# Kernel tuning notes

Measured on AMD Instinct MI355X. Metric: run time of the kernel, lower is better.

The kernel has to match this reference:

```python
import jax, jax.numpy as jnp
import numpy as np

B, L, D, H, F, NL = 112, 128, 768, 12, 3072, 3
E = D // H  # head dim = 64
BN_EPS = 1e-5


def _bn(x, gamma, beta):
    # torch BatchNorm1d applied on x.permute(0,2,1): per-channel (d_model) stats over batch+seq
    mean = jnp.mean(x, axis=(0, 1), keepdims=True)
    var = jnp.var(x, axis=(0, 1), keepdims=True)
    return (x - mean) * jax.lax.rsqrt(var + BN_EPS) * gamma + beta


def setup_inputs() -> dict:
    key = jax.random.key(0)
    ks = jax.random.split(key, 10)
    s = 0.02
    inp = {
        "x": jax.random.normal(ks[0], (B, L, D), jnp.float32),
        "attn_bias": jax.random.normal(ks[1], (B, L, L, H), jnp.float32) * 0.1,
        "Wq": jax.random.normal(ks[2], (NL, D, D), jnp.float32) * s,
        "bq": jnp.zeros((NL, D), jnp.float32),
        "Wk": jax.random.normal(ks[3], (NL, D, D), jnp.float32) * s,
        "bk": jnp.zeros((NL, D), jnp.float32),
        "Wv": jax.random.normal(ks[4], (NL, D, D), jnp.float32) * s,
        "bv": jnp.zeros((NL, D), jnp.float32),
        "Wo": jax.random.normal(ks[5], (NL, D, D), jnp.float32) * s,
        "bo": jnp.zeros((NL, D), jnp.float32),
        "W1": jax.random.normal(ks[6], (NL, F, D), jnp.float32) * s,  # conv1 k=1 == Linear
        "b1": jnp.zeros((NL, F), jnp.float32),
        "W2": jax.random.normal(ks[7], (NL, D, F), jnp.float32) * s,  # conv2 k=1 == Linear
        "b2": jnp.zeros((NL, D), jnp.float32),
        "g1": jnp.ones((NL, D), jnp.float32),
        "be1": jnp.zeros((NL, D), jnp.float32),
        "g2": jnp.ones((NL, D), jnp.float32),
        "be2": jnp.zeros((NL, D), jnp.float32),
        "gf": jnp.ones((D,), jnp.float32),
        "bef": jnp.zeros((D,), jnp.float32),
    }
    return inp


def reference(x, attn_bias, Wq, bq, Wk, bk, Wv, bv, Wo, bo,
              W1, b1, W2, b2, g1, be1, g2, be2, gf, bef):
    scale = 1.0 / float(np.sqrt(E))
    bias_bhls = jnp.transpose(attn_bias, (0, 3, 1, 2))  # [B,H,L,S]
    for l in range(NL):
        q = (x @ Wq[l].T + bq[l]).reshape(B, L, H, E)
        k = (x @ Wk[l].T + bk[l]).reshape(B, L, H, E)
        v = (x @ Wv[l].T + bv[l]).reshape(B, L, H, E)
        scores = jnp.einsum('blhe,bshe->bhls', q, k)  # O(L^2) score tensor
        A = jax.nn.softmax(scores * scale + bias_bhls, axis=-1)
        V = jnp.einsum('bhls,bshd->blhd', A, v).reshape(B, L, D)
        new_x = V @ Wo[l].T + bo[l]
        x = _bn(x + new_x, g1[l], be1[l])
        y = jax.nn.gelu(x @ W1[l].T + b1[l], approximate=False)
        y = y @ W2[l].T + b2[l]
        x = _bn(x + y, g2[l], be2[l])
    return _bn(x, gf, bef)  # Encoder final BatchNorm1d(d_model)
```

## Files before the change

### kernel.cpp

```cpp
#include <hip/hip_runtime.h>

#define NB 112
#define SEQ 128
#define DM 768
#define NH 12
#define HD 64
#define FF 3072
#define NLAYER 3
#define MTOK (NB*SEQ)
#define QKVN (3*DM)
#define HEADTOT (NB*NH)
#define QSZ ((size_t)HEADTOT*SEQ*HD)

typedef unsigned short u16;
typedef __attribute__((ext_vector_type(8))) short short8;
typedef __attribute__((ext_vector_type(4))) float f32x4;
typedef __attribute__((ext_vector_type(4))) unsigned short us4;

__device__ __forceinline__ u16 f2bf(float f){
  unsigned u = __builtin_bit_cast(unsigned, f);
  u += 0x7FFFu + ((u >> 16) & 1u);
  return (u16)(u >> 16);
}
__device__ __forceinline__ float bf2f(u16 b){
  unsigned u = ((unsigned)b) << 16;
  return __builtin_bit_cast(float, u);
}

__device__ __forceinline__ void gl_lds16(const void* g, void* l){
  __builtin_amdgcn_global_load_lds((const __attribute__((address_space(1))) unsigned*)g,
                                   (__attribute__((address_space(3))) unsigned*)l, 16, 0, 0);
}

template<int EPI>
__global__ __launch_bounds__(512, 2)
void gemm_bt(const u16* __restrict__ A, const u16* __restrict__ W,
             const float* __restrict__ bias, u16* __restrict__ obf,
             float* __restrict__ of32, const float* __restrict__ res,
             float* __restrict__ p1, float* __restrict__ p2,
             int M, int N, int K, int Nt, int TPB)
{
  __shared__ __align__(16) char smem[131072];
  const int tid = threadIdx.x;
  const int w = tid >> 6, lane = tid & 63;
  const int wm = w >> 2, wn = w & 3;
  const int fr = lane & 15, fg = lane >> 4;
  const int fko = fg * 8;
  const int grid = gridDim.x;
  const int q8 = grid >> 3, r8 = grid & 7;
  const int xcd = blockIdx.x & 7, pos = blockIdx.x >> 3;
  const int start = xcd < r8 ? xcd * (q8 + 1) : r8 * (q8 + 1) + (xcd - r8) * q8;
  const int swz = start + pos;
  const int nt = K >> 6;
  const int tot = TPB * nt;
  const int l3 = lane >> 3;
  const int k16s = ((lane & 7) ^ l3) * 8;
  int rowAK[2][2], rowBK[2][2];
  #pragma unroll
  for (int mh = 0; mh < 2; mh++)
    #pragma unroll
    for (int j = 0; j < 2; j++)
      rowAK[mh][j] = (mh*64 + j*128 + w*8 + l3) * K;
  #pragma unroll
  for (int h = 0; h < 2; h++)
    #pragma unroll
    for (int j = 0; j < 2; j++)
      rowBK[h][j] = (h*128 + (w + j*8)*8 + l3) * K;

  auto stA2 = [&](int bb, int mh, int soff) {
    const u16* g0 = A + (size_t)soff + rowAK[mh][0] + k16s;
    const u16* g1 = A + (size_t)soff + rowAK[mh][1] + k16s;
    char* d = smem + bb*65536 + (mh*64 + w*8)*128;
    gl_lds16(g0, d);
    gl_lds16(g1, d + 16384);
  };
  auto stB2 = [&](int bb, int h, int soff) {
    const u16* g0 = W + (size_t)soff + rowBK[h][0] + k16s;
    const u16* g1 = W + (size_t)soff + rowBK[h][1] + k16s;
    char* d = smem + bb*65536 + 32768 + (h*128 + w*8)*128;
    gl_lds16(g0, d);
    gl_lds16(g1, d + 8192);
  };
  const int axor = (fr & 7) << 4;
  auto rdA2 = [&](int bb, int mh, int kh, int mf) -> short8 {
    const int row = wm*128 + mh*64 + mf*16 + fr;
    return *(const short8*)(smem + bb*65536 + row*128 + (((kh*32 + fko)*2) ^ axor));
  };
  auto rdB2 = [&](int bb, int kh, int nf) -> short8 {
    const int row = wn*64 + nf*16 + fr;
    return *(const short8*)(smem + bb*65536 + 32768 + row*128 + (((kh*32 + fko)*2) ^ axor));
  };
  auto coord = [&](int r, int& bm, int& bn) {
    const int lin = swz * TPB + r;
    const int mI = lin / Nt;
    bm = mI * 256; bn = (lin - mI * Nt) * 256;
  };

  f32x4 acc[8][4] = {};

  auto epi = [&](int bm, int bn) {
    float bs[4] = {0,0,0,0}, bq[4] = {0,0,0,0};
    #pragma unroll
    for (int mi = 0; mi < 8; mi++) {
      #pragma unroll
      for (int ni = 0; ni < 4; ni++) {
        const int c = bn + wn*64 + ni*16 + fr;
        const int r0 = bm + wm*128 + (mi>>2)*64 + (mi&3)*16 + fg*4;
        const float bc = bias[c];
        #pragma unroll
        for (int j = 0; j < 4; j++) {
          float v = acc[mi][ni][j] + bc;
          const int r = r0 + j;
          if constexpr (EPI == 1) {
            v = 0.5f * v * (1.0f + erff(v * 0.70710678118654752f));
            obf[(size_t)r * N + c] = f2bf(v);
          } else if constexpr (EPI == 2) {
            const float y = v + res[(size_t)r * N + c];
            of32[(size_t)r * N + c] = y;
            bs[ni] += y; bq[ni] += y * y;
          } else {
            const int which = c / DM;
            const int cc = c - which * DM;
            const int hh = cc >> 6, e = cc & 63;
            const int bb = r >> 7, l = r & 127;
            obf[(size_t)which * QSZ + ((size_t)(bb*NH + hh) * SEQ + l) * HD + e] = f2bf(v);
          }
        }
        acc[mi][ni] = (f32x4){0.f, 0.f, 0.f, 0.f};
      }
    }
    if constexpr (EPI == 2) {
      const int mIdx = bm >> 8;
      #pragma unroll
      for (int ni = 0; ni < 4; ni++) {
        float s = bs[ni], qq = bq[ni];
        s  += __shfl_xor(s, 16);  s  += __shfl_xor(s, 32);
        qq += __shfl_xor(qq, 16); qq += __shfl_xor(qq, 32);
        if (fg == 0) {
          const int c = bn + wn*64 + ni*16 + fr;
          p1[(mIdx*2 + wm) * N + c] = s;
          p2[(mIdx*2 + wm) * N + c] = qq;
        }
      }
    }
  };

  int r0 = 0, kt0 = 0, bm0, bn0; coord(0, bm0, bn0);
  int r1 = 0, kt1 = 1, bm1 = bm0, bn1 = bn0;
  int r2 = 0, kt2 = 2, bm2 = bm0;
  if (kt2 >= nt) { kt2 -= nt; r2 = 1; int d; if (r2 < TPB) coord(r2, bm2, d); }

  stA2(0, 0, bm0*K); stA2(0, 1, bm0*K);
  stB2(0, 0, bn0*K); stB2(0, 1, bn0*K);
  if (tot > 1) stA2(1, 0, bm1*K + kt1*64);
  asm volatile("s_waitcnt vmcnt(2)" ::: "memory");
  __builtin_amdgcn_s_barrier();

  short8 bk0[4], bk1[4], av[4];
  for (int it = 0; it < tot; ++it) {
    const int bufc = it & 1, nb = bufc ^ 1;
    const bool st1 = (it + 1 < tot), st2 = (it + 2 < tot);
    const int sB1 = bn1*K + kt1*64;
    const int sA1 = bm1*K + kt1*64;
    const int sA2 = bm2*K + kt2*64;
    #pragma unroll
    for (int i = 0; i < 4; i++) av[i] = rdA2(bufc, 0, 0, i);
    #pragma unroll
    for (int i = 0; i < 4; i++) bk0[i] = rdB2(bufc, 0, i);
    if (st1) stB2(nb, 0, sB1);
    __builtin_amdgcn_s_barrier();
    asm volatile("s_waitcnt lgkmcnt(0)" ::: "memory");
    __builtin_amdgcn_sched_barrier(0);
    __builtin_amdgcn_s_setprio(1);
    #pragma unroll
    for (int mi = 0; mi < 4; mi++)
      #pragma unroll
      for (int ni = 0; ni < 4; ni++)
        acc[mi][ni] = __builtin_amdgcn_mfma_f32_16x16x32_bf16(av[mi], bk0[ni], acc[mi][ni], 0, 0, 0);
    __builtin_amdgcn_s_setprio(0);
    __builtin_amdgcn_s_barrier();
    #pragma unroll
    for (int i = 0; i < 4; i++) av[i] = rdA2(bufc, 0, 1, i);
    #pragma unroll
    for (int i = 0; i < 4; i++) bk1[i] = rdB2(bufc, 1, i);
    if (st1) stB2(nb, 1, sB1);
    __builtin_amdgcn_s_barrier();
    asm volatile("s_waitcnt lgkmcnt(0)" ::: "memory");
    __builtin_amdgcn_sched_barrier(0);
    __builtin_amdgcn_s_setprio(1);
    #pragma unroll
    for (int mi = 0; mi < 4; mi++)
      #pragma unroll
      for (int ni = 0; ni < 4; ni++)
        acc[mi][ni] = __builtin_amdgcn_mfma_f32_16x16x32_bf16(av[mi], bk1[ni], acc[mi][ni], 0, 0, 0);
    __builtin_amdgcn_s_setprio(0);
    if (st1) { asm volatile("s_waitcnt vmcnt(4)" ::: "memory"); }
    else     { asm volatile("s_waitcnt vmcnt(0)" ::: "memory"); }
    __builtin_amdgcn_s_barrier();
    #pragma unroll
    for (int i = 0; i < 4; i++) av[i] = rdA2(bufc, 1, 0, i);
    if (st2) stA2(bufc, 0, sA2);
    __builtin_amdgcn_s_barrier();
    asm volatile("s_waitcnt lgkmcnt(0)" ::: "memory");
    __builtin_amdgcn_sched_barrier(0);
    __builtin_amdgcn_s_setprio(1);
    #pragma unroll
    for (int mi = 0; mi < 4; mi++)
      #pragma unroll
      for (int ni = 0; ni < 4; ni++)
        acc[4+mi][ni] = __builtin_amdgcn_mfma_f32_16x16x32_bf16(av[mi], bk0[ni], acc[4+mi][ni], 0, 0, 0);
    __builtin_amdgcn_s_setprio(0);
    __builtin_amdgcn_s_barrier();
    #pragma unroll
    for (int i = 0; i < 4; i++) av[i] = rdA2(bufc, 1, 1, i);
    if (st1) stA2(nb, 1, sA1);
    __builtin_amdgcn_s_barrier();
    asm volatile("s_waitcnt lgkmcnt(0)" ::: "memory");
    __builtin_amdgcn_sched_barrier(0);
    __builtin_amdgcn_s_setprio(1);
    #pragma unroll
    for (int mi = 0; mi < 4; mi++)
      #pragma unroll
      for (int ni = 0; ni < 4; ni++)
        acc[4+mi][ni] = __builtin_amdgcn_mfma_f32_16x16x32_bf16(av[mi], bk1[ni], acc[4+mi][ni], 0, 0, 0);
    __builtin_amdgcn_s_setprio(0);
    if (st2)      { asm volatile("s_waitcnt vmcnt(4)" ::: "memory"); }
    else if (st1) { asm volatile("s_waitcnt vmcnt(2)" ::: "memory"); }
    __builtin_amdgcn_s_barrier();
    if (kt0 == nt - 1) {
      epi(bm0, bn0);
      kt0 = 0; r0++;
      if (r0 < TPB) coord(r0, bm0, bn0);
    } else kt0++;
    kt1++; if (kt1 == nt) { kt1 = 0; r1++; if (r1 < TPB) coord(r1, bm1, bn1); }
    kt2++; if (kt2 == nt) { kt2 = 0; r2++; if (r2 < TPB) { int d; coord(r2, bm2, d); } }
  }
}

__global__ __launch_bounds__(256)
void attn_kernel(const u16* __restrict__ qkvb, const u16* __restrict__ biasT,
                 u16* __restrict__ ab)
{
  const int h = blockIdx.x, b = blockIdx.y;
  const int tid = threadIdx.x, w = tid >> 6, lane = tid & 63;
  const int bh = b * NH + h;
  const u16* qp = qkvb + (size_t)bh * SEQ * HD;
  const u16* kp = qkvb + QSZ + (size_t)bh * SEQ * HD;
  const u16* vp = qkvb + 2 * QSZ + (size_t)bh * SEQ * HD;
  __shared__ __align__(16) u16 vT[HD * 136];
  __shared__ __align__(16) u16 P[SEQ * 136];
  {
    const int s = tid & 127, half = tid >> 7;
    #pragma unroll
    for (int rr = 0; rr < 4; rr++) {
      const int e0 = half * 32 + rr * 8;
      short8 v8 = *(const short8*)&vp[s * HD + e0];
      #pragma unroll
      for (int j = 0; j < 8; j++) vT[(e0 + j) * 136 + s] = (u16)v8[j];
    }
  }
  const int fr = lane & 15, fg = lane >> 4;
  f32x4 sacc[2][8] = {};
  #pragma unroll
  for (int ks = 0; ks < 2; ks++) {
    const int k0 = ks * 32 + fg * 8;
    short8 qf[2], kf[8];
    #pragma unroll
    for (int mi = 0; mi < 2; mi++) qf[mi] = *(const short8*)&qp[(w*32 + mi*16 + fr) * HD + k0];
    #pragma unroll
    for (int ni = 0; ni < 8; ni++) kf[ni] = *(const short8*)&kp[(ni*16 + fr) * HD + k0];
    #pragma unroll
    for (int mi = 0; mi < 2; mi++)
      #pragma unroll
      for (int ni = 0; ni < 8; ni++)
        sacc[mi][ni] = __builtin_amdgcn_mfma_f32_16x16x32_bf16(qf[mi], kf[ni], sacc[mi][ni], 0, 0, 0);
  }
  const u16* bt = biasT + (size_t)bh * SEQ * SEQ;
  #pragma unroll
  for (int mi = 0; mi < 2; mi++) {
    #pragma unroll
    for (int j = 0; j < 4; j++) {
      const int l = w*32 + mi*16 + fg*4 + j;
      float vals[8];
      float mx = -1e30f;
      #pragma unroll
      for (int ni = 0; ni < 8; ni++) {
        vals[ni] = sacc[mi][ni][j] * 0.125f + bf2f(bt[l * SEQ + ni*16 + fr]);
        mx = fmaxf(mx, vals[ni]);
      }
      #pragma unroll
      for (int d = 1; d < 16; d <<= 1) mx = fmaxf(mx, __shfl_xor(mx, d));
      float sum = 0.f;
      #pragma unroll
      for (int ni = 0; ni < 8; ni++) { vals[ni] = __expf(vals[ni] - mx); sum += vals[ni]; }
      #pragma unroll
      for (int d = 1; d < 16; d <<= 1) sum += __shfl_xor(sum, d);
      const float inv = 1.0f / sum;
      #pragma unroll
      for (int ni = 0; ni < 8; ni++) P[l * 136 + ni*16 + fr] = f2bf(vals[ni] * inv);
    }
  }
  __syncthreads();
  f32x4 oacc[2][4] = {};
  #pragma unroll
  for (int ss = 0; ss < 4; ss++) {
    const int s0 = ss * 32 + fg * 8;
    short8 pf[2], vf[4];
    #pragma unroll
    for (int mi = 0; mi < 2; mi++) pf[mi] = *(const short8*)&P[(w*32 + mi*16 + fr) * 136 + s0];
    #pragma unroll
    for (int ei = 0; ei < 4; ei++) vf[ei] = *(const short8*)&vT[(ei*16 + fr) * 136 + s0];
    #pragma unroll
    for (int mi = 0; mi < 2; mi++)
      #pragma unroll
      for (int ei = 0; ei < 4; ei++)
        oacc[mi][ei] = __builtin_amdgcn_mfma_f32_16x16x32_bf16(pf[mi], vf[ei], oacc[mi][ei], 0, 0, 0);
  }
  #pragma unroll
  for (int mi = 0; mi < 2; mi++)
    #pragma unroll
    for (int ei = 0; ei < 4; ei++)
      #pragma unroll
      for (int j = 0; j < 4; j++) {
        const int r = b * SEQ + w*32 + mi*16 + fg*4 + j;
        const int c = h * HD + ei*16 + fr;
        ab[(size_t)r * DM + c] = f2bf(oacc[mi][ei][j]);
      }
}

template<bool FINAL>
__global__ __launch_bounds__(256)
void bn_final(const float* __restrict__ p1, const float* __restrict__ p2,
              const float* __restrict__ ga, const float* __restrict__ be,
              const float* __restrict__ gb, const float* __restrict__ beb,
              float* __restrict__ sc, float* __restrict__ sh)
{
  const int c = blockIdx.x * 256 + threadIdx.x;
  float s = 0, q = 0;
  for (int i = 0; i < 112; i++) { s += p1[i * DM + c]; q += p2[i * DM + c]; }
  const float mean = s * (1.0f / MTOK);
  const float var = q * (1.0f / MTOK) - mean * mean;
  const float rstd = rsqrtf(var + 1e-5f);
  if constexpr (!FINAL) {
    const float g = ga[c] * rstd;
    sc[c] = g;
    sh[c] = be[c] - mean * g;
  } else {
    const float sc2 = ga[c] * rstd;
    const float sh2 = be[c] - mean * sc2;
    const float varf = sc2 * sc2 * var;
    const float meanf = sc2 * mean + sh2;
    const float scf = gb[c] * rsqrtf(varf + 1e-5f);
    const float shf = beb[c] - meanf * scf;
    sc[c] = scf * sc2;
    sh[c] = scf * sh2 + shf;
  }
}

__global__ __launch_bounds__(256)
void bn_apply(const float* __restrict__ xi, const float* __restrict__ sc,
              const float* __restrict__ sh, float* __restrict__ xo, u16* __restrict__ xb)
{
  const int i = blockIdx.x * 256 + threadIdx.x;
  const int cv = i % (DM / 4);
  float4 v = ((const float4*)xi)[i];
  const float4 s = ((const float4*)sc)[cv];
  const float4 h = ((const float4*)sh)[cv];
  float4 y;
  y.x = v.x * s.x + h.x; y.y = v.y * s.y + h.y;
  y.z = v.z * s.z + h.z; y.w = v.w * s.w + h.w;
  ((float4*)xo)[i] = y;
  if (xb) {
    us4 pk; pk[0] = f2bf(y.x); pk[1] = f2bf(y.y); pk[2] = f2bf(y.z); pk[3] = f2bf(y.w);
    *(us4*)(xb + (size_t)i * 4) = pk;
  }
}

__global__ __launch_bounds__(256)
void init_x(const float* __restrict__ xi, float* __restrict__ xo, u16* __restrict__ xb)
{
  const int i = blockIdx.x * 256 + threadIdx.x;
  float4 v = ((const float4*)xi)[i];
  ((float4*)xo)[i] = v;
  us4 pk; pk[0] = f2bf(v.x); pk[1] = f2bf(v.y); pk[2] = f2bf(v.z); pk[3] = f2bf(v.w);
  *(us4*)(xb + (size_t)i * 4) = pk;
}

__global__ __launch_bounds__(256)
void conv_bf16(const float* __restrict__ s, u16* __restrict__ d, int n4)
{
  const int i = blockIdx.x * 256 + threadIdx.x;
  if (i >= n4) return;
  float4 v = ((const float4*)s)[i];
  us4 pk; pk[0] = f2bf(v.x); pk[1] = f2bf(v.y); pk[2] = f2bf(v.z); pk[3] = f2bf(v.w);
  *(us4*)(d + (size_t)i * 4) = pk;
}

__global__ __launch_bounds__(256)
void conv_qkvw(const float* __restrict__ wq, const float* __restrict__ wk,
               const float* __restrict__ wv, u16* __restrict__ d)
{
  const int i = blockIdx.x * 256 + threadIdx.x;
  const int per = QKVN * DM / 4;
  const int l = i / per;
  const int rem = i - l * per;
  const int r = rem / (DM / 4);
  const int cv = rem - r * (DM / 4);
  const float* srcrow;
  if (r < DM)          srcrow = wq + ((size_t)l * DM + r) * DM;
  else if (r < 2 * DM) srcrow = wk + ((size_t)l * DM + (r - DM)) * DM;
  else                 srcrow = wv + ((size_t)l * DM + (r - 2 * DM)) * DM;
  float4 v = ((const float4*)srcrow)[cv];
  us4 pk; pk[0] = f2bf(v.x); pk[1] = f2bf(v.y); pk[2] = f2bf(v.z); pk[3] = f2bf(v.w);
  *(us4*)(d + (size_t)i * 4) = pk;
}

__global__ __launch_bounds__(256)
void conv_bias_qkv(const float* __restrict__ bq, const float* __restrict__ bk,
                   const float* __restrict__ bv, float* __restrict__ d)
{
  const int i = blockIdx.x * 256 + threadIdx.x;
  const int l = i / QKVN;
  const int r = i - l * QKVN;
  float v;
  if (r < DM)          v = bq[l * DM + r];
  else if (r < 2 * DM) v = bk[l * DM + r - DM];
  else                 v = bv[l * DM + r - 2 * DM];
  d[i] = v;
}

__global__ __launch_bounds__(256)
void bias_tr(const float* __restrict__ src, u16* __restrict__ dst)
{
  const int l = blockIdx.x, b = blockIdx.y;
  __shared__ float row[SEQ * NH];
  const float* s = src + ((size_t)b * SEQ + l) * SEQ * NH;
  for (int i = threadIdx.x; i < SEQ * NH; i += 256) row[i] = s[i];
  __syncthreads();
  for (int i = threadIdx.x; i < SEQ * NH; i += 256) {
    const int h = i >> 7, ss = i & 127;
    dst[((size_t)(b * NH + h) * SEQ + l) * SEQ + ss] = f2bf(row[ss * NH + h]);
  }
}

extern "C" void kernel_launch(void* const* d_in, const int* in_sizes, int n_in,
                              void* d_out, int out_size, void* d_ws, size_t ws_size,
                              hipStream_t stream)
{
  const float* x    = (const float*)d_in[0];
  const float* abia = (const float*)d_in[1];
  const float* Wq   = (const float*)d_in[2];
  const float* bq   = (const float*)d_in[3];
  const float* Wk   = (const float*)d_in[4];
  const float* bk   = (const float*)d_in[5];
  const float* Wv   = (const float*)d_in[6];
  const float* bv   = (const float*)d_in[7];
  const float* Wo   = (const float*)d_in[8];
  const float* bo   = (const float*)d_in[9];
  const float* W1   = (const float*)d_in[10];
  const float* b1   = (const float*)d_in[11];
  const float* W2   = (const float*)d_in[12];
  const float* b2   = (const float*)d_in[13];
  const float* g1   = (const float*)d_in[14];
  const float* be1  = (const float*)d_in[15];
  const float* g2   = (const float*)d_in[16];
  const float* be2  = (const float*)d_in[17];
  const float* gf   = (const float*)d_in[18];
  const float* bef  = (const float*)d_in[19];
  float* out = (float*)d_out;

  char* ws = (char*)d_ws;
  size_t off = 0;
  auto alloc = [&](size_t n) -> char* {
    char* p = ws + off;
    off = (off + n + 255) & ~(size_t)255;
    return p;
  };
  u16*  wqkv  = (u16*)alloc((size_t)3 * QKVN * DM * 2);
  u16*  wo    = (u16*)alloc((size_t)3 * DM * DM * 2);
  u16*  w1    = (u16*)alloc((size_t)3 * FF * DM * 2);
  u16*  w2    = (u16*)alloc((size_t)3 * DM * FF * 2);
  float* bqkv = (float*)alloc((size_t)3 * QKVN * 4);
  u16*  xb    = (u16*)alloc((size_t)MTOK * DM * 2);
  u16*  ab    = (u16*)alloc((size_t)MTOK * DM * 2);
  u16*  big   = (u16*)alloc((size_t)MTOK * FF * 2);
  u16*  biasT = (u16*)alloc((size_t)HEADTOT * SEQ * SEQ * 2);
  float* p1   = (float*)alloc((size_t)112 * DM * 4);
  float* p2   = (float*)alloc((size_t)112 * DM * 4);
  float* sc   = (float*)alloc(DM * 4);
  float* sh   = (float*)alloc(DM * 4);
  if (off > ws_size) return;

  conv_qkvw<<<5184, 256, 0, stream>>>(Wq, Wk, Wv, wqkv);
  conv_bf16<<<1728, 256, 0, stream>>>(Wo, wo, 3 * DM * DM / 4);
  conv_bf16<<<6912, 256, 0, stream>>>(W1, w1, 3 * FF * DM / 4);
  conv_bf16<<<6912, 256, 0, stream>>>(W2, w2, 3 * DM * FF / 4);
  conv_bias_qkv<<<27, 256, 0, stream>>>(bq, bk, bv, bqkv);
  bias_tr<<<dim3(SEQ, NB), 256, 0, stream>>>(abia, biasT);
  init_x<<<MTOK * DM / 4 / 256, 256, 0, stream>>>(x, out, xb);

  auto gemm = [&](int epi, const u16* Ap, const u16* Wp, const float* bp,
                  u16* ob, float* o32, const float* rs, int M, int N, int K) {
    const int Nt = N / 256;
    const int tiles = (M / 256) * Nt;
    const int tpb = (tiles + 255) / 256;
    const int grid = tiles / tpb;
    if (epi == 1)
      gemm_bt<1><<<grid, 512, 0, stream>>>(Ap, Wp, bp, ob, o32, rs, p1, p2, M, N, K, Nt, tpb);
    else if (epi == 2)
      gemm_bt<2><<<grid, 512, 0, stream>>>(Ap, Wp, bp, ob, o32, rs, p1, p2, M, N, K, Nt, tpb);
    else
      gemm_bt<3><<<grid, 512, 0, stream>>>(Ap, Wp, bp, ob, o32, rs, p1, p2, M, N, K, Nt, tpb);
  };

  for (int l = 0; l < NLAYER; l++) {
    gemm(3, xb, wqkv + (size_t)l * QKVN * DM, bqkv + l * QKVN, big, nullptr, nullptr,
         MTOK, QKVN, DM);
    attn_kernel<<<dim3(NH, NB), 256, 0, stream>>>(big, biasT, ab);
    gemm(2, ab, wo + (size_t)l * DM * DM, bo + l * DM, nullptr, out, out,
         MTOK, DM, DM);
    bn_final<false><<<3, 256, 0, stream>>>(p1, p2, g1 + l * DM, be1 + l * DM,
                                           nullptr, nullptr, sc, sh);
    bn_apply<<<MTOK * DM / 4 / 256, 256, 0, stream>>>(out, sc, sh, out, xb);
    gemm(1, xb, w1 + (size_t)l * FF * DM, b1 + l * FF, big, nullptr, nullptr,
         MTOK, FF, DM);
    gemm(2, big, w2 + (size_t)l * DM * FF, b2 + l * DM, nullptr, out, out,
         MTOK, DM, FF);
    if (l < NLAYER - 1) {
      bn_final<false><<<3, 256, 0, stream>>>(p1, p2, g2 + l * DM, be2 + l * DM,
                                             nullptr, nullptr, sc, sh);
      bn_apply<<<MTOK * DM / 4 / 256, 256, 0, stream>>>(out, sc, sh, out, xb);
    } else {
      bn_final<true><<<3, 256, 0, stream>>>(p1, p2, g2 + l * DM, be2 + l * DM,
                                            gf, bef, sc, sh);
      bn_apply<<<MTOK * DM / 4 / 256, 256, 0, stream>>>(out, sc, sh, out, nullptr);
    }
  }
}
```

Baseline: 1.255 ms.

## Keep residual in bf16, use tanh GELU and packed bf16 conversion in epilogues

Residual adds now read the bf16 activation copy instead of an fp32 copy. The bn_apply passes therefore write only bf16 (fp32 only at the end), and the fp32 init copy is dropped. The FFN1 epilogue swaps exact erf GELU for a sigmoid-form tanh approximation, and the epilogues use the packed v_cvt_pk_bf16_f32 instruction. This cuts memory traffic and epilogue ALU work, at the cost of reduced residual precision and an approximate GELU.

Measured after the change: 1.172 ms. 1.07x faster.

```diff
diff --git a/kernel.cpp b/kernel.cpp
--- a/kernel.cpp
+++ b/kernel.cpp
@@ -26,6 +26,15 @@
   unsigned u = ((unsigned)b) << 16;
   return __builtin_bit_cast(float, u);
 }
+__device__ __forceinline__ unsigned cvt_pk_bf16(float lo, float hi){
+  unsigned r;
+  asm("v_cvt_pk_bf16_f32 %0, %1, %2" : "=v"(r) : "v"(lo), "v"(hi));
+  return r;
+}
+__device__ __forceinline__ float gelu_t(float x){
+  const float t = -1.5957691216057308f * x * __builtin_fmaf(0.044715f, x*x, 1.0f);
+  return __fdividef(x, 1.0f + __expf(t));
+}
 
 __device__ __forceinline__ void gl_lds16(const void* g, void* l){
   __builtin_amdgcn_global_load_lds((const __attribute__((address_space(1))) unsigned*)g,
@@ -36,7 +45,7 @@
 __global__ __launch_bounds__(512, 2)
 void gemm_bt(const u16* __restrict__ A, const u16* __restrict__ W,
              const float* __restrict__ bias, u16* __restrict__ obf,
-             float* __restrict__ of32, const float* __restrict__ res,
+             float* __restrict__ of32, const u16* __restrict__ res,
              float* __restrict__ p1, float* __restrict__ p2,
              int M, int N, int K, int Nt, int TPB)
 {
@@ -107,24 +116,34 @@
         const int c = bn + wn*64 + ni*16 + fr;
         const int r0 = bm + wm*128 + (mi>>2)*64 + (mi&3)*16 + fg*4;
         const float bc = bias[c];
+        float v[4];
         #pragma unroll
-        for (int j = 0; j < 4; j++) {
-          float v = acc[mi][ni][j] + bc;
-          const int r = r0 + j;
-          if constexpr (EPI == 1) {
-            v = 0.5f * v * (1.0f + erff(v * 0.70710678118654752f));
-            obf[(size_t)r * N + c] = f2bf(v);
-          } else if constexpr (EPI == 2) {
-            const float y = v + res[(size_t)r * N + c];
-            of32[(size_t)r * N + c] = y;
+        for (int j = 0; j < 4; j++) v[j] = acc[mi][ni][j] + bc;
+        if constexpr (EPI == 1) {
+          #pragma unroll
+          for (int j = 0; j < 4; j++) v[j] = gelu_t(v[j]);
+          const unsigned p01 = cvt_pk_bf16(v[0], v[1]);
+          const unsigned p23 = cvt_pk_bf16(v[2], v[3]);
+          u16* d = obf + (size_t)r0 * N + c;
+          d[0] = (u16)p01; d[N] = (u16)(p01 >> 16);
+          d[2*N] = (u16)p23; d[3*N] = (u16)(p23 >> 16);
+        } else if constexpr (EPI == 2) {
+          #pragma unroll
+          for (int j = 0; j < 4; j++) {
+            const float y = v[j] + bf2f(res[(size_t)(r0+j) * N + c]);
+            of32[(size_t)(r0+j) * N + c] = y;
             bs[ni] += y; bq[ni] += y * y;
-          } else {
-            const int which = c / DM;
-            const int cc = c - which * DM;
-            const int hh = cc >> 6, e = cc & 63;
-            const int bb = r >> 7, l = r & 127;
-            obf[(size_t)which * QSZ + ((size_t)(bb*NH + hh) * SEQ + l) * HD + e] = f2bf(v);
           }
+        } else {
+          const int which = c / DM;
+          const int cc = c - which * DM;
+          const int hh = cc >> 6, e = cc & 63;
+          const int bb = r0 >> 7, l = r0 & 127;
+          const unsigned p01 = cvt_pk_bf16(v[0], v[1]);
+          const unsigned p23 = cvt_pk_bf16(v[2], v[3]);
+          u16* d = obf + (size_t)which * QSZ + ((size_t)(bb*NH + hh) * SEQ + l) * HD + e;
+          d[0] = (u16)p01; d[HD] = (u16)(p01 >> 16);
+          d[2*HD] = (u16)p23; d[3*HD] = (u16)(p23 >> 16);
         }
         acc[mi][ni] = (f32x4){0.f, 0.f, 0.f, 0.f};
       }
@@ -357,6 +376,7 @@
   }
 }
 
+template<int MODE>
 __global__ __launch_bounds__(256)
 void bn_apply(const float* __restrict__ xi, const float* __restrict__ sc,
               const float* __restrict__ sh, float* __restrict__ xo, u16* __restrict__ xb)
@@ -369,21 +389,12 @@
   float4 y;
   y.x = v.x * s.x + h.x; y.y = v.y * s.y + h.y;
   y.z = v.z * s.z + h.z; y.w = v.w * s.w + h.w;
-  ((float4*)xo)[i] = y;
-  if (xb) {
+  if constexpr (MODE == 1) {
+    ((float4*)xo)[i] = y;
+  } else {
     us4 pk; pk[0] = f2bf(y.x); pk[1] = f2bf(y.y); pk[2] = f2bf(y.z); pk[3] = f2bf(y.w);
     *(us4*)(xb + (size_t)i * 4) = pk;
   }
-}
-
-__global__ __launch_bounds__(256)
-void init_x(const float* __restrict__ xi, float* __restrict__ xo, u16* __restrict__ xb)
-{
-  const int i = blockIdx.x * 256 + threadIdx.x;
-  float4 v = ((const float4*)xi)[i];
-  ((float4*)xo)[i] = v;
-  us4 pk; pk[0] = f2bf(v.x); pk[1] = f2bf(v.y); pk[2] = f2bf(v.z); pk[3] = f2bf(v.w);
-  *(us4*)(xb + (size_t)i * 4) = pk;
 }
 
 __global__ __launch_bounds__(256)
@@ -497,10 +508,10 @@
   conv_bf16<<<6912, 256, 0, stream>>>(W2, w2, 3 * DM * FF / 4);
   conv_bias_qkv<<<27, 256, 0, stream>>>(bq, bk, bv, bqkv);
   bias_tr<<<dim3(SEQ, NB), 256, 0, stream>>>(abia, biasT);
-  init_x<<<MTOK * DM / 4 / 256, 256, 0, stream>>>(x, out, xb);
+  conv_bf16<<<MTOK * DM / 4 / 256, 256, 0, stream>>>(x, xb, MTOK * DM / 4);
 
   auto gemm = [&](int epi, const u16* Ap, const u16* Wp, const float* bp,
-                  u16* ob, float* o32, const float* rs, int M, int N, int K) {
+                  u16* ob, float* o32, const u16* rs, int M, int N, int K) {
     const int Nt = N / 256;
     const int tiles = (M / 256) * Nt;
     const int tpb = (tiles + 255) / 256;
@@ -517,23 +528,23 @@
     gemm(3, xb, wqkv + (size_t)l * QKVN * DM, bqkv + l * QKVN, big, nullptr, nullptr,
          MTOK, QKVN, DM);
     attn_kernel<<<dim3(NH, NB), 256, 0, stream>>>(big, biasT, ab);
-    gemm(2, ab, wo + (size_t)l * DM * DM, bo + l * DM, nullptr, out, out,
+    gemm(2, ab, wo + (size_t)l * DM * DM, bo + l * DM, nullptr, out, xb,
          MTOK, DM, DM);
     bn_final<false><<<3, 256, 0, stream>>>(p1, p2, g1 + l * DM, be1 + l * DM,
                                            nullptr, nullptr, sc, sh);
-    bn_apply<<<MTOK * DM / 4 / 256, 256, 0, stream>>>(out, sc, sh, out, xb);
+    bn_apply<0><<<MTOK * DM / 4 / 256, 256, 0, stream>>>(out, sc, sh, nullptr, xb);
     gemm(1, xb, w1 + (size_t)l * FF * DM, b1 + l * FF, big, nullptr, nullptr,
          MTOK, FF, DM);
-    gemm(2, big, w2 + (size_t)l * DM * FF, b2 + l * DM, nullptr, out, out,
+    gemm(2, big, w2 + (size_t)l * DM * FF, b2 + l * DM, nullptr, out, xb,
          MTOK, DM, FF);
     if (l < NLAYER - 1) {
       bn_final<false><<<3, 256, 0, stream>>>(p1, p2, g2 + l * DM, be2 + l * DM,
                                              nullptr, nullptr, sc, sh);
-      bn_apply<<<MTOK * DM / 4 / 256, 256, 0, stream>>>(out, sc, sh, out, xb);
+      bn_apply<0><<<MTOK * DM / 4 / 256, 256, 0, stream>>>(out, sc, sh, nullptr, xb);
     } else {
       bn_final<true><<<3, 256, 0, stream>>>(p1, p2, g2 + l * DM, be2 + l * DM,
                                             gf, bef, sc, sh);
-      bn_apply<<<MTOK * DM / 4 / 256, 256, 0, stream>>>(out, sc, sh, out, nullptr);
+      bn_apply<1><<<MTOK * DM / 4 / 256, 256, 0, stream>>>(out, sc, sh, out, nullptr);
     }
   }
 }
```
